# Kernel optimization log

Measured on AMD Instinct MI355X. Metric: run time of the kernel, lower is better.

Reference implementation:

```python
import jax, jax.numpy as jnp
import numpy as np

LN_EPS = 1e-5

def _layernorm(x, gamma, beta):
    mu = jnp.mean(x, axis=-1, keepdims=True)
    var = jnp.mean((x - mu) ** 2, axis=-1, keepdims=True)
    return (x - mu) / jnp.sqrt(var + LN_EPS) * gamma + beta

def setup_inputs() -> dict:
    key = jax.random.key(0)
    ks = jax.random.split(key, 12)
    B, S, D, V, H = 2, 2048, 1024, 32000, 16
    d_ff = 4 * D
    inp = {}
    inp["V"] = jax.random.randint(ks[0], (B, S), 0, V, dtype=jnp.int64)
    inp["num_heads"] = H
    sc = 0.02
    inp["emb"] = jax.random.normal(ks[1], (V, D), dtype=jnp.float32) * sc
    inp["w_o"] = jax.random.normal(ks[2], (D, D), dtype=jnp.float32) * sc
    inp["w1"] = jax.random.normal(ks[3], (D, d_ff), dtype=jnp.float32) * sc
    inp["b1"] = jnp.zeros((d_ff,), dtype=jnp.float32)
    inp["w2"] = jax.random.normal(ks[4], (d_ff, D), dtype=jnp.float32) * sc
    inp["b2"] = jnp.zeros((D,), dtype=jnp.float32)
    inp["gamma1"] = jnp.ones((D,), dtype=jnp.float32)
    inp["beta1"] = jnp.zeros((D,), dtype=jnp.float32)
    inp["gamma2"] = jnp.ones((D,), dtype=jnp.float32)
    inp["beta2"] = jnp.zeros((D,), dtype=jnp.float32)
    return inp

def reference(V, num_heads, emb, w_o, w1, b1, w2, b2, gamma1, beta1, gamma2, beta2):
    # Embedding lookup: [B, S, D]
    x = emb[V]
    B, S, D = x.shape
    hd = D // num_heads
    # NOTE: the original forward never applies w_q/w_k/w_v -- q=k=v=embedding,
    # split per head along the feature dim.
    qh = x.reshape(B, S, num_heads, hd)
    scores = jnp.einsum("bqhd,bkhd->bhqk", qh, qh) / jnp.sqrt(jnp.float32(hd))
    attn = jax.nn.softmax(scores, axis=-1)
    ctx = jnp.einsum("bhqk,bkhd->bqhd", attn, qh).reshape(B, S, D)
    attn_out = ctx @ w_o
    x1 = _layernorm(x + attn_out, gamma1, beta1)
    ff = jax.nn.relu(x1 @ w1 + b1) @ w2 + b2
    return _layernorm(x1 + ff, gamma2, beta2)
```

## Files before the change

kernel.cpp:

```cpp
#include <hip/hip_runtime.h>
#include <hip/hip_bf16.h>

#define B_  2
#define S_  2048
#define D_  1024
#define H_  16
#define HD_ 64
#define DFF 4096
#define NT  (B_ * S_)

typedef __bf16 bf16;
typedef __bf16 bf16x8 __attribute__((ext_vector_type(8)));
typedef __bf16 bf16x4 __attribute__((ext_vector_type(4)));
typedef __bf16 bf16x2 __attribute__((ext_vector_type(2)));
typedef float  f32x4  __attribute__((ext_vector_type(4)));
typedef float  f32x16 __attribute__((ext_vector_type(16)));
typedef int    i32x2  __attribute__((ext_vector_type(2)));

typedef const __attribute__((address_space(1))) unsigned int GLB_U32;
typedef __attribute__((address_space(3))) unsigned int AS3_U32;

__device__ __forceinline__ void gload16(const void* g, void* l) {
    __builtin_amdgcn_global_load_lds((GLB_U32*)g, (AS3_U32*)l, 16, 0, 0);
}

#define MFMA32(A, B, C) __builtin_amdgcn_mfma_f32_32x32x16_bf16(A, B, C, 0, 0, 0)
#define MFMA16(A, B, C) __builtin_amdgcn_mfma_f32_16x16x32_bf16(A, B, C, 0, 0, 0)

__device__ __forceinline__ unsigned pk2(float a, float b) {
    union { bf16x2 v; unsigned u; } t;
    t.v[0] = (bf16)a; t.v[1] = (bf16)b;
    return t.u;
}

#define ATT_SCL 0.18033688011112042f

#define PREP_EMB  (B_ * (S_ / 32) * (D_ / 32))
#define PREP_WO   ((D_ / 32) * (D_ / 32))
#define PREP_W1   ((D_ / 32) * (DFF / 32))
#define PREP_W2   ((DFF / 32) * (D_ / 32))
#define PREP_TOT  (PREP_EMB + PREP_WO + PREP_W1 + PREP_W2)

__device__ __forceinline__ void transcvt_tile(const float* src, bf16* dst,
                                              int R, int C, int tile,
                                              float* tf, int tx, int ty) {
    int tiles_c = C >> 5;
    int r0 = (tile / tiles_c) << 5;
    int c0 = (tile % tiles_c) << 5;
#pragma unroll
    for (int i = 0; i < 4; i++)
        tf[(ty + i * 8) * 33 + tx] = src[(size_t)(r0 + ty + i * 8) * C + c0 + tx];
    __syncthreads();
#pragma unroll
    for (int i = 0; i < 4; i++)
        dst[(size_t)(c0 + ty + i * 8) * R + r0 + tx] = (bf16)tf[tx * 33 + ty + i * 8];
}

__global__ __launch_bounds__(256)
void k_prep(const int* __restrict__ V, const float* __restrict__ emb,
            bf16* __restrict__ xb, bf16* __restrict__ xT,
            const float* __restrict__ w_o, bf16* __restrict__ wobT,
            const float* __restrict__ w1, bf16* __restrict__ w1T,
            const float* __restrict__ w2, bf16* __restrict__ w2T) {
    __shared__ float tf[32 * 33];
    int bidx = blockIdx.x;
    int tx = threadIdx.x & 31, ty = threadIdx.x >> 5;

    if (bidx < PREP_EMB) {
        bf16* tb = (bf16*)tf;
        const int tiles_d = D_ / 32;
        int b   = bidx / ((S_ / 32) * tiles_d);
        int rem = bidx % ((S_ / 32) * tiles_d);
        int ts = rem / tiles_d, td = rem % tiles_d;
        int s0 = ts * 32, d0 = td * 32;
        bf16* xbb = xb + (size_t)b * S_ * D_;
        bf16* dst = xT + (size_t)b * D_ * S_;
#pragma unroll
        for (int i = 0; i < 4; i++) {
            int srow = s0 + ty + i * 8;
            int vid = V[b * S_ + srow];
            bf16 val = (bf16)emb[(size_t)vid * D_ + d0 + tx];
            xbb[(size_t)srow * D_ + d0 + tx] = val;
            tb[(ty + i * 8) * 34 + tx] = val;
        }
        __syncthreads();
#pragma unroll
        for (int i = 0; i < 4; i++)
            dst[(size_t)(d0 + ty + i * 8) * S_ + s0 + tx] = tb[tx * 34 + ty + i * 8];
    } else if (bidx < PREP_EMB + PREP_WO) {
        transcvt_tile(w_o, wobT, D_, D_, bidx - PREP_EMB, tf, tx, ty);
    } else if (bidx < PREP_EMB + PREP_WO + PREP_W1) {
        transcvt_tile(w1, w1T, D_, DFF, bidx - PREP_EMB - PREP_WO, tf, tx, ty);
    } else {
        transcvt_tile(w2, w2T, DFF, D_, bidx - PREP_EMB - PREP_WO - PREP_W1, tf, tx, ty);
    }
}

__global__ __launch_bounds__(256)
void k_attn(const bf16* __restrict__ xb, const bf16* __restrict__ xT,
            bf16* __restrict__ ctxb) {
    __shared__ alignas(16) bf16 Kt[2][64][64];
    __shared__ alignas(16) bf16 Vt[2][64][64];

    int bh = blockIdx.x >> 4;
    int qt = blockIdx.x & 15;
    int b = bh >> 4, h = bh & 15;
    int tid = threadIdx.x;
    int w = tid >> 6, lane = tid & 63;
    int l31 = lane & 31, hi = lane >> 5;

    const bf16* xq = xb + (size_t)b * S_ * D_ + h * HD_;
    const bf16* vT = xT + ((size_t)b * D_ + h * HD_) * S_;

    int q0 = qt * 128 + w * 32;

    bf16x8 qf[4];
#pragma unroll
    for (int c = 0; c < 4; c++) {
        qf[c] = *(const bf16x8*)(xq + (size_t)(q0 + l31) * D_ + c * 16 + hi * 8);
#pragma unroll
        for (int i = 0; i < 8; i++)
            qf[c][i] = (bf16)((float)qf[c][i] * ATT_SCL);
    }

    bf16x8 onesf;
#pragma unroll
    for (int i = 0; i < 8; i++) onesf[i] = (bf16)1.0f;

    int srow = tid >> 3;
    int sbyx = ((tid & 7) << 4) ^ ((srow & 7) << 4);

    const char* kg = (const char*)(xq + (size_t)srow * D_) + sbyx;
    const char* vg = (const char*)(vT + (size_t)srow * S_) + sbyx;
    char* kd0 = (char*)&Kt[0][0][0] + tid * 16;
    char* vd0 = (char*)&Vt[0][0][0] + tid * 16;
    char* kd1 = (char*)&Kt[1][0][0] + tid * 16;
    char* vd1 = (char*)&Vt[1][0][0] + tid * 16;

    f32x16 o0 = {}, o1 = {}, ol = {};

    const int KSTR = 64 * D_ * 2;
    const int VSTR = 64 * 2;
    const int NTILES = S_ / 64;

    gload16(kg, kd0); gload16(kg + 32 * D_ * 2, kd0 + 4096);
    gload16(vg, vd0); gload16(vg + 32 * S_ * 2, vd0 + 4096);
    kg += KSTR; vg += VSTR;

    int rsw = (l31 & 7) << 4;
    const char* KbA = (const char*)&Kt[0][0][0] + l31 * 128;
    const char* KbB = (const char*)&Kt[1][0][0] + l31 * 128;
    const char* VbA = (const char*)&Vt[0][0][0] + l31 * 128;
    const char* VbB = (const char*)&Vt[1][0][0] + l31 * 128;

    for (int kt = 0; kt < NTILES; kt++) {
        __syncthreads();
        if (kt + 1 < NTILES) {
            char* kd = (kt & 1) ? kd0 : kd1;
            char* vd = (kt & 1) ? vd0 : vd1;
            gload16(kg, kd); gload16(kg + 32 * D_ * 2, kd + 4096);
            gload16(vg, vd); gload16(vg + 32 * S_ * 2, vd + 4096);
            kg += KSTR; vg += VSTR;
        }
        const char* Kb = (kt & 1) ? KbB : KbA;
        const char* Vb = (kt & 1) ? VbB : VbA;

        f32x16 sa0 = {}, sa1 = {};
        {
            bf16x8 kf0[4], kf1[4];
#pragma unroll
            for (int c = 0; c < 4; c++) {
                int by = (c * 32 + hi * 16) ^ rsw;
                kf0[c] = *(const bf16x8*)(Kb + by);
                kf1[c] = *(const bf16x8*)(Kb + 32 * 128 + by);
            }
            __builtin_amdgcn_s_setprio(1);
#pragma unroll
            for (int c = 0; c < 4; c++) sa0 = MFMA32(kf0[c], qf[c], sa0);
#pragma unroll
            for (int c = 0; c < 4; c++) sa1 = MFMA32(kf1[c], qf[c], sa1);
            __builtin_amdgcn_s_setprio(0);
        }

        float p0[16], p1[16];
#pragma unroll
        for (int i = 0; i < 16; i++) p0[i] = exp2f(sa0[i]);
#pragma unroll
        for (int i = 0; i < 16; i++) p1[i] = exp2f(sa1[i]);

        union { unsigned u[4]; bf16x8 v; } pfA0, pfA1, pfB0, pfB1;
        {
            unsigned a0 = pk2(p0[0],  p0[1]),  a1 = pk2(p0[2],  p0[3]);
            unsigned a2 = pk2(p0[4],  p0[5]),  a3 = pk2(p0[6],  p0[7]);
            unsigned a4 = pk2(p0[8],  p0[9]),  a5 = pk2(p0[10], p0[11]);
            unsigned a6 = pk2(p0[12], p0[13]), a7 = pk2(p0[14], p0[15]);
            i32x2 r;
            r = __builtin_amdgcn_permlane32_swap((int)a0, (int)a2, false, false);
            pfA0.u[0] = r[0]; pfA0.u[2] = r[1];
            r = __builtin_amdgcn_permlane32_swap((int)a1, (int)a3, false, false);
            pfA0.u[1] = r[0]; pfA0.u[3] = r[1];
            r = __builtin_amdgcn_permlane32_swap((int)a4, (int)a6, false, false);
            pfA1.u[0] = r[0]; pfA1.u[2] = r[1];
            r = __builtin_amdgcn_permlane32_swap((int)a5, (int)a7, false, false);
            pfA1.u[1] = r[0]; pfA1.u[3] = r[1];
        }
        {
            unsigned a0 = pk2(p1[0],  p1[1]),  a1 = pk2(p1[2],  p1[3]);
            unsigned a2 = pk2(p1[4],  p1[5]),  a3 = pk2(p1[6],  p1[7]);
            unsigned a4 = pk2(p1[8],  p1[9]),  a5 = pk2(p1[10], p1[11]);
            unsigned a6 = pk2(p1[12], p1[13]), a7 = pk2(p1[14], p1[15]);
            i32x2 r;
            r = __builtin_amdgcn_permlane32_swap((int)a0, (int)a2, false, false);
            pfB0.u[0] = r[0]; pfB0.u[2] = r[1];
            r = __builtin_amdgcn_permlane32_swap((int)a1, (int)a3, false, false);
            pfB0.u[1] = r[0]; pfB0.u[3] = r[1];
            r = __builtin_amdgcn_permlane32_swap((int)a4, (int)a6, false, false);
            pfB1.u[0] = r[0]; pfB1.u[2] = r[1];
            r = __builtin_amdgcn_permlane32_swap((int)a5, (int)a7, false, false);
            pfB1.u[1] = r[0]; pfB1.u[3] = r[1];
        }

        {
            bf16x8 v0, v1, v2, v3;
            v0 = *(const bf16x8*)(Vb + ((0  + hi * 16) ^ rsw));
            v1 = *(const bf16x8*)(Vb + ((32 + hi * 16) ^ rsw));
            v2 = *(const bf16x8*)(Vb + ((64 + hi * 16) ^ rsw));
            v3 = *(const bf16x8*)(Vb + ((96 + hi * 16) ^ rsw));
            __builtin_amdgcn_s_setprio(1);
            o0 = MFMA32(v0, pfA0.v, o0);
            o0 = MFMA32(v1, pfA1.v, o0);
            o0 = MFMA32(v2, pfB0.v, o0);
            o0 = MFMA32(v3, pfB1.v, o0);
            ol = MFMA32(onesf, pfA0.v, ol);
            ol = MFMA32(onesf, pfA1.v, ol);
            __builtin_amdgcn_s_setprio(0);
            v0 = *(const bf16x8*)(Vb + 32 * 128 + ((0  + hi * 16) ^ rsw));
            v1 = *(const bf16x8*)(Vb + 32 * 128 + ((32 + hi * 16) ^ rsw));
            v2 = *(const bf16x8*)(Vb + 32 * 128 + ((64 + hi * 16) ^ rsw));
            v3 = *(const bf16x8*)(Vb + 32 * 128 + ((96 + hi * 16) ^ rsw));
            __builtin_amdgcn_s_setprio(1);
            o1 = MFMA32(v0, pfA0.v, o1);
            o1 = MFMA32(v1, pfA1.v, o1);
            o1 = MFMA32(v2, pfB0.v, o1);
            o1 = MFMA32(v3, pfB1.v, o1);
            ol = MFMA32(onesf, pfB0.v, ol);
            ol = MFMA32(onesf, pfB1.v, ol);
            __builtin_amdgcn_s_setprio(0);
        }
    }

    float rinv = 1.0f / ol[0];
    int q = q0 + l31;
    bf16* crow = ctxb + ((size_t)b * S_ + q) * D_ + h * HD_;
#pragma unroll
    for (int g = 0; g < 4; g++) {
        bf16x4 ov;
#pragma unroll
        for (int j = 0; j < 4; j++) ov[j] = (bf16)(o0[4 * g + j] * rinv);
        *(bf16x4*)(crow + 8 * g + 4 * hi) = ov;
    }
#pragma unroll
    for (int g = 0; g < 4; g++) {
        bf16x4 ov;
#pragma unroll
        for (int j = 0; j < 4; j++) ov[j] = (bf16)(o1[4 * g + j] * rinv);
        *(bf16x4*)(crow + 32 + 8 * g + 4 * hi) = ov;
    }
}

template <int BIAS, int RELU, int OUT_MODE>
__global__ __launch_bounds__(512)
void k_gemm256(const bf16* __restrict__ A, const bf16* __restrict__ Bt,
               const float* __restrict__ bias,
               float* __restrict__ outf, bf16* __restrict__ outb,
               int M, int N, int K) {
    __shared__ alignas(16) bf16 As[2][256][64];
    __shared__ alignas(16) bf16 Bs[2][256][64];

    int ntn = N >> 8;
    int m0 = (int)(blockIdx.x / ntn) << 8;
    int n0 = (int)(blockIdx.x % ntn) << 8;
    int tid = threadIdx.x;
    int lane = tid & 63, w = tid >> 6;
    int wm = w >> 2, wn = w & 3;
    int l15 = lane & 15, lhi = lane >> 4;
    int NK = K >> 6;

    int r0 = tid >> 3;
    int sbyx = ((tid & 7) << 4) ^ ((r0 & 7) << 4);
    const char* ag = (const char*)(A  + (size_t)(m0 + r0) * K) + sbyx;
    const char* bg = (const char*)(Bt + (size_t)(n0 + r0) * K) + sbyx;
    const size_t r64 = (size_t)64 * K * 2;

    auto stA = [&](int ob, size_t ko, int half) {
        char* d = (char*)&As[ob][0][0] + half * 16384 + tid * 16;
        gload16(ag + ko + (size_t)(2 * half) * r64, d);
        gload16(ag + ko + (size_t)(2 * half + 1) * r64, d + 8192);
    };
    auto stB = [&](int ob, size_t ko, int half) {
        char* d = (char*)&Bs[ob][0][0] + half * 16384 + tid * 16;
        gload16(bg + ko + (size_t)(2 * half) * r64, d);
        gload16(bg + ko + (size_t)(2 * half + 1) * r64, d + 8192);
    };

    stA(0, 0, 0); stA(0, 0, 1); stB(0, 0, 0); stB(0, 0, 1);

    f32x4 acc[8][4] = {};
    int rsw = (l15 & 7) << 4;
    int aro = (wm * 128 + l15) * 128;
    int bro = (wn * 64 + l15) * 128;

    for (int t = 0; t < NK; t++) {
        int buf = t & 1, ob = buf ^ 1;
        size_t ko = (size_t)(t + 1) * 128;
        const char* aB = (const char*)&As[buf][0][0] + aro;
        const char* bB = (const char*)&Bs[buf][0][0] + bro;
        bf16x8 af[4][2], bfr[4][2];

        if (t + 1 < NK) {
            stA(ob, ko, 0); stA(ob, ko, 1);
            asm volatile("s_waitcnt vmcnt(4)" ::: "memory");
        } else {
            asm volatile("s_waitcnt vmcnt(0)" ::: "memory");
        }
        __builtin_amdgcn_s_barrier();
        __builtin_amdgcn_sched_barrier(0);
#pragma unroll
        for (int mi = 0; mi < 4; mi++) {
            af[mi][0] = *(const bf16x8*)(aB + mi * 2048 + ((lhi * 16) ^ rsw));
            af[mi][1] = *(const bf16x8*)(aB + mi * 2048 + ((64 + lhi * 16) ^ rsw));
        }
#pragma unroll
        for (int ni = 0; ni < 2; ni++) {
            bfr[ni][0] = *(const bf16x8*)(bB + ni * 2048 + ((lhi * 16) ^ rsw));
            bfr[ni][1] = *(const bf16x8*)(bB + ni * 2048 + ((64 + lhi * 16) ^ rsw));
        }
        __builtin_amdgcn_s_setprio(1);
#pragma unroll
        for (int mi = 0; mi < 4; mi++)
#pragma unroll
            for (int ni = 0; ni < 2; ni++) {
                acc[mi][ni] = MFMA16(af[mi][0], bfr[ni][0], acc[mi][ni]);
                acc[mi][ni] = MFMA16(af[mi][1], bfr[ni][1], acc[mi][ni]);
            }
        __builtin_amdgcn_s_setprio(0);
        __builtin_amdgcn_s_barrier();

#pragma unroll
        for (int ni = 2; ni < 4; ni++) {
            bfr[ni][0] = *(const bf16x8*)(bB + ni * 2048 + ((lhi * 16) ^ rsw));
            bfr[ni][1] = *(const bf16x8*)(bB + ni * 2048 + ((64 + lhi * 16) ^ rsw));
        }
        if (t + 1 < NK) { stB(ob, ko, 0); stB(ob, ko, 1); }
        __builtin_amdgcn_s_barrier();
        __builtin_amdgcn_s_setprio(1);
#pragma unroll
        for (int mi = 0; mi < 4; mi++)
#pragma unroll
            for (int ni = 2; ni < 4; ni++) {
                acc[mi][ni] = MFMA16(af[mi][0], bfr[ni][0], acc[mi][ni]);
                acc[mi][ni] = MFMA16(af[mi][1], bfr[ni][1], acc[mi][ni]);
            }
        __builtin_amdgcn_s_setprio(0);
        __builtin_amdgcn_s_barrier();

#pragma unroll
        for (int mi = 0; mi < 4; mi++) {
            af[mi][0] = *(const bf16x8*)(aB + (4 + mi) * 2048 + ((lhi * 16) ^ rsw));
            af[mi][1] = *(const bf16x8*)(aB + (4 + mi) * 2048 + ((64 + lhi * 16) ^ rsw));
        }
        __builtin_amdgcn_s_barrier();
        __builtin_amdgcn_s_setprio(1);
#pragma unroll
        for (int mi = 0; mi < 4; mi++)
#pragma unroll
            for (int ni = 0; ni < 2; ni++) {
                acc[4 + mi][ni] = MFMA16(af[mi][0], bfr[ni][0], acc[4 + mi][ni]);
                acc[4 + mi][ni] = MFMA16(af[mi][1], bfr[ni][1], acc[4 + mi][ni]);
            }
        __builtin_amdgcn_s_setprio(0);
        __builtin_amdgcn_s_barrier();

        __builtin_amdgcn_s_barrier();
        __builtin_amdgcn_s_setprio(1);
#pragma unroll
        for (int mi = 0; mi < 4; mi++)
#pragma unroll
            for (int ni = 2; ni < 4; ni++) {
                acc[4 + mi][ni] = MFMA16(af[mi][0], bfr[ni][0], acc[4 + mi][ni]);
                acc[4 + mi][ni] = MFMA16(af[mi][1], bfr[ni][1], acc[4 + mi][ni]);
            }
        __builtin_amdgcn_s_setprio(0);
        __builtin_amdgcn_s_barrier();
    }

#pragma unroll
    for (int mi = 0; mi < 8; mi++) {
        int grow = m0 + wm * 128 + mi * 16 + lhi * 4;
#pragma unroll
        for (int ni = 0; ni < 4; ni++) {
            int gcol = n0 + wn * 64 + ni * 16 + l15;
            float bv = BIAS ? bias[gcol] : 0.f;
#pragma unroll
            for (int r = 0; r < 4; r++) {
                float v = acc[mi][ni][r] + bv;
                if (RELU) v = fmaxf(v, 0.f);
                size_t idx = (size_t)(grow + r) * N + gcol;
                if (OUT_MODE & 1) outf[idx] = v;
                if (OUT_MODE & 2) outb[idx] = (bf16)v;
            }
        }
    }
}

template <int BIAS, int RELU, int OUT_MODE, int SPLITK>
__global__ __launch_bounds__(512)
void k_gemm8(const bf16* __restrict__ A, const bf16* __restrict__ Bt,
             const float* __restrict__ bias,
             float* __restrict__ outf, bf16* __restrict__ outb,
             int M, int N, int K) {
    __shared__ alignas(16) bf16 As[2][256][64];
    __shared__ alignas(16) bf16 Bs[2][128][64];

    int ntn = N >> 7;
    int m0 = (int)(blockIdx.x / ntn) << 8;
    int n0 = (int)(blockIdx.x % ntn) << 7;
    int tid = threadIdx.x;
    int lane = tid & 63;
    int w = tid >> 6;
    int wm = w >> 1, wn = w & 1;
    int l15 = lane & 15, lhi = lane >> 4;

    int Ks = K / SPLITK;
    int NK = Ks >> 6;
    size_t kbase = (size_t)blockIdx.y * Ks;
    float* outp = outf + (size_t)blockIdx.y * M * N;

    int srow = tid >> 3;
    int sbyx = ((tid & 7) << 4) ^ ((srow & 7) << 4);
    const char* ag = (const char*)(A  + (size_t)(m0 + srow) * K + kbase) + sbyx;
    const char* bg = (const char*)(Bt + (size_t)(n0 + srow) * K + kbase) + sbyx;
    const size_t r64 = (size_t)64 * K * 2;

    auto stageA0 = [&](int ob, size_t ko) {
        char* d = (char*)&As[ob][0][0] + tid * 16;
        gload16(ag + ko, d);
        gload16(ag + ko + r64, d + 8192);
    };
    auto stageA1 = [&](int ob, size_t ko) {
        char* d = (char*)&As[ob][0][0] + tid * 16 + 16384;
        gload16(ag + ko + 2 * r64, d);
        gload16(ag + ko + 3 * r64, d + 8192);
    };
    auto stageB = [&](int ob, size_t ko) {
        char* d = (char*)&Bs[ob][0][0] + tid * 16;
        gload16(bg + ko, d);
        gload16(bg + ko + r64, d + 8192);
    };

    stageA0(0, 0); stageA1(0, 0); stageB(0, 0);

    f32x4 acc[4][4] = {};
    int rsw = (l15 & 7) << 4;
    int aro = (wm * 64 + l15) * 128;
    int bro = (wn * 64 + l15) * 128;

    for (int t = 0; t < NK; t++) {
        int buf = t & 1, ob = buf ^ 1;
        size_t ko = (size_t)(t + 1) * 128;
        const char* aB = (const char*)&As[buf][0][0] + aro;
        const char* bB = (const char*)&Bs[buf][0][0] + bro;
        bf16x8 af[4][2], bn[2];

        if (t + 1 < NK) {
            stageA0(ob, ko);
            asm volatile("s_waitcnt vmcnt(2)" ::: "memory");
        } else {
            asm volatile("s_waitcnt vmcnt(0)" ::: "memory");
        }
        __builtin_amdgcn_s_barrier();
#pragma unroll
        for (int m = 0; m < 4; m++) {
            af[m][0] = *(const bf16x8*)(aB + m * 2048 + ((lhi * 16) ^ rsw));
            af[m][1] = *(const bf16x8*)(aB + m * 2048 + ((64 + lhi * 16) ^ rsw));
        }
        bn[0] = *(const bf16x8*)(bB + ((lhi * 16) ^ rsw));
        bn[1] = *(const bf16x8*)(bB + ((64 + lhi * 16) ^ rsw));
        __builtin_amdgcn_s_setprio(1);
#pragma unroll
        for (int m = 0; m < 4; m++) {
            acc[m][0] = MFMA16(af[m][0], bn[0], acc[m][0]);
            acc[m][0] = MFMA16(af[m][1], bn[1], acc[m][0]);
        }
        __builtin_amdgcn_s_setprio(0);
        __builtin_amdgcn_s_barrier();

        bn[0] = *(const bf16x8*)(bB + 2048 + ((lhi * 16) ^ rsw));
        bn[1] = *(const bf16x8*)(bB + 2048 + ((64 + lhi * 16) ^ rsw));
        if (t + 1 < NK) stageA1(ob, ko);
        __builtin_amdgcn_s_barrier();
        __builtin_amdgcn_s_setprio(1);
#pragma unroll
        for (int m = 0; m < 4; m++) {
            acc[m][1] = MFMA16(af[m][0], bn[0], acc[m][1]);
            acc[m][1] = MFMA16(af[m][1], bn[1], acc[m][1]);
        }
        __builtin_amdgcn_s_setprio(0);
        __builtin_amdgcn_s_barrier();

        bn[0] = *(const bf16x8*)(bB + 2 * 2048 + ((lhi * 16) ^ rsw));
        bn[1] = *(const bf16x8*)(bB + 2 * 2048 + ((64 + lhi * 16) ^ rsw));
        if (t + 1 < NK) stageB(ob, ko);
        __builtin_amdgcn_s_barrier();
        __builtin_amdgcn_s_setprio(1);
#pragma unroll
        for (int m = 0; m < 4; m++) {
            acc[m][2] = MFMA16(af[m][0], bn[0], acc[m][2]);
            acc[m][2] = MFMA16(af[m][1], bn[1], acc[m][2]);
        }
        __builtin_amdgcn_s_setprio(0);
        __builtin_amdgcn_s_barrier();

        bn[0] = *(const bf16x8*)(bB + 3 * 2048 + ((lhi * 16) ^ rsw));
        bn[1] = *(const bf16x8*)(bB + 3 * 2048 + ((64 + lhi * 16) ^ rsw));
        __builtin_amdgcn_s_barrier();
        __builtin_amdgcn_s_setprio(1);
#pragma unroll
        for (int m = 0; m < 4; m++) {
            acc[m][3] = MFMA16(af[m][0], bn[0], acc[m][3]);
            acc[m][3] = MFMA16(af[m][1], bn[1], acc[m][3]);
        }
        __builtin_amdgcn_s_setprio(0);
        __builtin_amdgcn_s_barrier();
    }

#pragma unroll
    for (int m = 0; m < 4; m++) {
        int grow = m0 + wm * 64 + m * 16 + lhi * 4;
#pragma unroll
        for (int n = 0; n < 4; n++) {
            int gcol = n0 + wn * 64 + n * 16 + l15;
            float bv = BIAS ? bias[gcol] : 0.f;
#pragma unroll
            for (int r = 0; r < 4; r++) {
                float v = acc[m][n][r] + bv;
                if (RELU) v = fmaxf(v, 0.f);
                size_t idx = (size_t)(grow + r) * N + gcol;
                if (OUT_MODE & 1) outp[idx] = v;
                if (OUT_MODE & 2) outb[idx] = (bf16)v;
            }
        }
    }
}

template <int BIAS, int RELU, int OUT_MODE, int SPLITK>
__global__ __launch_bounds__(256)
void k_gemm(const bf16* __restrict__ A, const bf16* __restrict__ Bt,
            const float* __restrict__ bias,
            float* __restrict__ outf, bf16* __restrict__ outb,
            int M, int N, int K) {
    __shared__ alignas(16) bf16 As[128][32];
    __shared__ alignas(16) bf16 Bs[128][32];

    int nb_n = N >> 7;
    int m0 = (blockIdx.x / nb_n) << 7;
    int n0 = (blockIdx.x % nb_n) << 7;
    int tid = threadIdx.x;
    int w = tid >> 6, lane = tid & 63;
    int wr = (w >> 1) << 6, wc = (w & 1) << 6;
    int l15 = lane & 15, lhi = lane >> 4;

    int srow = w * 16 + (lane >> 2);
    int scol = (lane & 3) << 3;

    int Ks = K / SPLITK;
    int kbase = blockIdx.y * Ks;
    float* outp = outf + (size_t)blockIdx.y * M * N;

    f32x4 acc[4][4] = {};

    for (int k0 = kbase; k0 < kbase + Ks; k0 += 32) {
        gload16(A  + (size_t)(m0 + srow) * K + k0 + scol,      &As[srow][scol]);
        gload16(A  + (size_t)(m0 + 64 + srow) * K + k0 + scol, &As[64 + srow][scol]);
        gload16(Bt + (size_t)(n0 + srow) * K + k0 + scol,      &Bs[srow][scol]);
        gload16(Bt + (size_t)(n0 + 64 + srow) * K + k0 + scol, &Bs[64 + srow][scol]);
        __syncthreads();
        bf16x8 af[4], bfr[4];
#pragma unroll
        for (int mi = 0; mi < 4; mi++)
            af[mi] = *(const bf16x8*)&As[wr + mi * 16 + l15][lhi * 8];
#pragma unroll
        for (int ni = 0; ni < 4; ni++)
            bfr[ni] = *(const bf16x8*)&Bs[wc + ni * 16 + l15][lhi * 8];
#pragma unroll
        for (int mi = 0; mi < 4; mi++)
#pragma unroll
            for (int ni = 0; ni < 4; ni++)
                acc[mi][ni] = MFMA16(af[mi], bfr[ni], acc[mi][ni]);
        __syncthreads();
    }

#pragma unroll
    for (int mi = 0; mi < 4; mi++) {
        int grow = m0 + wr + mi * 16 + lhi * 4;
#pragma unroll
        for (int ni = 0; ni < 4; ni++) {
            int gcol = n0 + wc + ni * 16 + l15;
            float bv = BIAS ? bias[gcol] : 0.f;
#pragma unroll
            for (int r = 0; r < 4; r++) {
                float v = acc[mi][ni][r] + bv;
                if (RELU) v = fmaxf(v, 0.f);
                size_t idx = (size_t)(grow + r) * N + gcol;
                if (OUT_MODE & 1) outp[idx] = v;
                if (OUT_MODE & 2) outb[idx] = (bf16)v;
            }
        }
    }
}

__global__ __launch_bounds__(256)
void k_ln1(const float* __restrict__ pA, const bf16* __restrict__ resb,
           const float* __restrict__ gamma, const float* __restrict__ beta,
           bf16* __restrict__ x1b) {
    const float* pB = pA + (size_t)NT * D_;
    int row = blockIdx.x, tid = threadIdx.x;
    size_t base = (size_t)row * D_ + tid * 4;
    float4 a = *(const float4*)(pA + base);
    float4 c = *(const float4*)(pB + base);
    bf16x4 rb = *(const bf16x4*)(resb + base);
    float4 v;
    v.x = a.x + c.x + (float)rb[0];
    v.y = a.y + c.y + (float)rb[1];
    v.z = a.z + c.z + (float)rb[2];
    v.w = a.w + c.w + (float)rb[3];
    float s  = v.x + v.y + v.z + v.w;
    float sq = v.x * v.x + v.y * v.y + v.z * v.z + v.w * v.w;
#pragma unroll
    for (int m = 1; m < 64; m <<= 1) {
        s  += __shfl_xor(s, m, 64);
        sq += __shfl_xor(sq, m, 64);
    }
    __shared__ float ss[4], ssq[4];
    int w = tid >> 6;
    if ((tid & 63) == 0) { ss[w] = s; ssq[w] = sq; }
    __syncthreads();
    s  = ss[0] + ss[1] + ss[2] + ss[3];
    sq = ssq[0] + ssq[1] + ssq[2] + ssq[3];
    float mu  = s * (1.f / D_);
    float var = sq * (1.f / D_) - mu * mu;
    float rstd = rsqrtf(var + 1e-5f);
    float4 g  = *(const float4*)(gamma + tid * 4);
    float4 bt = *(const float4*)(beta + tid * 4);
    bf16x4 ob;
    ob[0] = (bf16)((v.x - mu) * rstd * g.x + bt.x);
    ob[1] = (bf16)((v.y - mu) * rstd * g.y + bt.y);
    ob[2] = (bf16)((v.z - mu) * rstd * g.z + bt.z);
    ob[3] = (bf16)((v.w - mu) * rstd * g.w + bt.w);
    *(bf16x4*)(x1b + base) = ob;
}

__global__ __launch_bounds__(256)
void k_ln2(const float* __restrict__ pA, const float* __restrict__ bias,
           const bf16* __restrict__ resb,
           const float* __restrict__ gamma, const float* __restrict__ beta,
           float* __restrict__ out) {
    const float* pB = pA + (size_t)NT * D_;
    int row = blockIdx.x, tid = threadIdx.x;
    size_t base = (size_t)row * D_ + tid * 4;
    float4 a = *(const float4*)(pA + base);
    float4 c = *(const float4*)(pB + base);
    bf16x4 rb = *(const bf16x4*)(resb + base);
    float4 bb = *(const float4*)(bias + tid * 4);
    float4 v;
    v.x = a.x + c.x + (float)rb[0] + bb.x;
    v.y = a.y + c.y + (float)rb[1] + bb.y;
    v.z = a.z + c.z + (float)rb[2] + bb.z;
    v.w = a.w + c.w + (float)rb[3] + bb.w;
    float s  = v.x + v.y + v.z + v.w;
    float sq = v.x * v.x + v.y * v.y + v.z * v.z + v.w * v.w;
#pragma unroll
    for (int m = 1; m < 64; m <<= 1) {
        s  += __shfl_xor(s, m, 64);
        sq += __shfl_xor(sq, m, 64);
    }
    __shared__ float ss[4], ssq[4];
    int w = tid >> 6;
    if ((tid & 63) == 0) { ss[w] = s; ssq[w] = sq; }
    __syncthreads();
    s  = ss[0] + ss[1] + ss[2] + ss[3];
    sq = ssq[0] + ssq[1] + ssq[2] + ssq[3];
    float mu  = s * (1.f / D_);
    float var = sq * (1.f / D_) - mu * mu;
    float rstd = rsqrtf(var + 1e-5f);
    float4 g  = *(const float4*)(gamma + tid * 4);
    float4 bt = *(const float4*)(beta + tid * 4);
    float4 o;
    o.x = (v.x - mu) * rstd * g.x + bt.x;
    o.y = (v.y - mu) * rstd * g.y + bt.y;
    o.z = (v.z - mu) * rstd * g.z + bt.z;
    o.w = (v.w - mu) * rstd * g.w + bt.w;
    *(float4*)(out + base) = o;
}

extern "C" void kernel_launch(void* const* d_in, const int* in_sizes, int n_in,
                              void* d_out, int out_size, void* d_ws, size_t ws_size,
                              hipStream_t stream) {
    const int*   Vi  = (const int*)d_in[0];
    const float* emb = (const float*)d_in[2];
    const float* w_o = (const float*)d_in[3];
    const float* w1  = (const float*)d_in[4];
    const float* b1  = (const float*)d_in[5];
    const float* w2  = (const float*)d_in[6];
    const float* b2  = (const float*)d_in[7];
    const float* g1  = (const float*)d_in[8];
    const float* be1 = (const float*)d_in[9];
    const float* g2  = (const float*)d_in[10];
    const float* be2 = (const float*)d_in[11];
    float* out = (float*)d_out;

    char* ws = (char*)d_ws;
    size_t off = 0;
    auto alloc = [&](size_t bytes) -> void* {
        void* p = ws + off;
        off += (bytes + 255) & ~(size_t)255;
        return p;
    };
    bf16*  xb   = (bf16*)alloc((size_t)NT * D_ * 2);
    bf16*  xT   = (bf16*)alloc((size_t)NT * D_ * 2);
    bf16*  wobT = (bf16*)alloc((size_t)D_ * D_ * 2);
    bf16*  w1T  = (bf16*)alloc((size_t)DFF * D_ * 2);
    bf16*  w2T  = (bf16*)alloc((size_t)D_ * DFF * 2);
    bf16*  ctxb = (bf16*)alloc((size_t)NT * D_ * 2);
    bf16*  x1b  = (bf16*)alloc((size_t)NT * D_ * 2);
    bf16*  h1   = (bf16*)alloc((size_t)NT * DFF * 2);
    float* RB   = (float*)alloc((size_t)2 * NT * D_ * 4);
    float* g1p  = RB;
    float* g3p  = RB;

    k_prep<<<PREP_TOT, 256, 0, stream>>>(Vi, emb, xb, xT, w_o, wobT, w1, w1T, w2, w2T);

    k_attn<<<32 * (S_ / 128), 256, 0, stream>>>(xb, xT, ctxb);

    k_gemm<0, 0, 1, 2><<<dim3((NT / 128) * (D_ / 128), 2), 256, 0, stream>>>(
        ctxb, wobT, nullptr, g1p, nullptr, NT, D_, D_);
    k_ln1<<<NT, 256, 0, stream>>>(g1p, xb, g1, be1, x1b);

    k_gemm256<1, 1, 2><<<(NT / 256) * (DFF / 256), 512, 0, stream>>>(
        x1b, w1T, b1, nullptr, h1, NT, DFF, D_);

    k_gemm8<0, 0, 1, 2><<<dim3((NT / 256) * (D_ / 128), 2), 512, 0, stream>>>(
        h1, w2T, nullptr, g3p, nullptr, NT, D_, DFF);
    k_ln2<<<NT, 256, 0, stream>>>(g3p, b2, x1b, g2, be2, out);
}
```

Before: 215.5 us.

## Triple-buffer attention K/V tiles and unify GEMM kernels into two-phase pipeline

The attention kernel moves from double to triple buffering of K/V tiles. It prefetches two tiles ahead and waits with explicit vmcnt instead of a full __syncthreads, to hide more global-load latency. The 512-thread GEMM is restructured from four barrier phases per k-step into two: A loads in one phase and B in the other, with all 16 MFMAs per half-k. The old 128x128 GEMM for the w_o projection is removed, so that projection now uses the same 256x128 kernel. The extra LDS for attention and the larger tile for the w_o GEMM may lower occupancy or leave CUs idle, since that GEMM now has fewer blocks.

```diff
diff --git a/kernel.cpp b/kernel.cpp
--- a/kernel.cpp
+++ b/kernel.cpp
@@ -99,8 +99,8 @@
 __global__ __launch_bounds__(256)
 void k_attn(const bf16* __restrict__ xb, const bf16* __restrict__ xT,
             bf16* __restrict__ ctxb) {
-    __shared__ alignas(16) bf16 Kt[2][64][64];
-    __shared__ alignas(16) bf16 Vt[2][64][64];
+    __shared__ alignas(16) bf16 Kt[3][64][64];
+    __shared__ alignas(16) bf16 Vt[3][64][64];
 
     int bh = blockIdx.x >> 4;
     int qt = blockIdx.x & 15;
@@ -132,38 +132,46 @@
 
     const char* kg = (const char*)(xq + (size_t)srow * D_) + sbyx;
     const char* vg = (const char*)(vT + (size_t)srow * S_) + sbyx;
-    char* kd0 = (char*)&Kt[0][0][0] + tid * 16;
-    char* vd0 = (char*)&Vt[0][0][0] + tid * 16;
-    char* kd1 = (char*)&Kt[1][0][0] + tid * 16;
-    char* vd1 = (char*)&Vt[1][0][0] + tid * 16;
-
-    f32x16 o0 = {}, o1 = {}, ol = {};
+
+    char* kdA = (char*)&Kt[0][0][0] + tid * 16;
+    char* kdB = (char*)&Kt[1][0][0] + tid * 16;
+    char* kdC = (char*)&Kt[2][0][0] + tid * 16;
+    char* vdA = (char*)&Vt[0][0][0] + tid * 16;
+    char* vdB = (char*)&Vt[1][0][0] + tid * 16;
+    char* vdC = (char*)&Vt[2][0][0] + tid * 16;
 
     const int KSTR = 64 * D_ * 2;
     const int VSTR = 64 * 2;
     const int NTILES = S_ / 64;
 
-    gload16(kg, kd0); gload16(kg + 32 * D_ * 2, kd0 + 4096);
-    gload16(vg, vd0); gload16(vg + 32 * S_ * 2, vd0 + 4096);
-    kg += KSTR; vg += VSTR;
+    auto stage = [&](char* kd, char* vd) {
+        gload16(kg, kd); gload16(kg + 32 * D_ * 2, kd + 4096);
+        gload16(vg, vd); gload16(vg + 32 * S_ * 2, vd + 4096);
+        kg += KSTR; vg += VSTR;
+    };
+
+    stage(kdA, vdA);
+    stage(kdB, vdB);
 
     int rsw = (l31 & 7) << 4;
-    const char* KbA = (const char*)&Kt[0][0][0] + l31 * 128;
-    const char* KbB = (const char*)&Kt[1][0][0] + l31 * 128;
-    const char* VbA = (const char*)&Vt[0][0][0] + l31 * 128;
-    const char* VbB = (const char*)&Vt[1][0][0] + l31 * 128;
+    const char* KrA = (const char*)&Kt[0][0][0] + l31 * 128;
+    const char* KrB = (const char*)&Kt[1][0][0] + l31 * 128;
+    const char* KrC = (const char*)&Kt[2][0][0] + l31 * 128;
+    const char* VrA = (const char*)&Vt[0][0][0] + l31 * 128;
+    const char* VrB = (const char*)&Vt[1][0][0] + l31 * 128;
+    const char* VrC = (const char*)&Vt[2][0][0] + l31 * 128;
+
+    f32x16 o0 = {}, o1 = {}, ol = {};
 
     for (int kt = 0; kt < NTILES; kt++) {
-        __syncthreads();
-        if (kt + 1 < NTILES) {
-            char* kd = (kt & 1) ? kd0 : kd1;
-            char* vd = (kt & 1) ? vd0 : vd1;
-            gload16(kg, kd); gload16(kg + 32 * D_ * 2, kd + 4096);
-            gload16(vg, vd); gload16(vg + 32 * S_ * 2, vd + 4096);
-            kg += KSTR; vg += VSTR;
-        }
-        const char* Kb = (kt & 1) ? KbB : KbA;
-        const char* Vb = (kt & 1) ? VbB : VbA;
+        if (kt == NTILES - 1) asm volatile("s_waitcnt vmcnt(0)" ::: "memory");
+        else                  asm volatile("s_waitcnt vmcnt(4)" ::: "memory");
+        __builtin_amdgcn_s_barrier();
+        __builtin_amdgcn_sched_barrier(0);
+        if (kt + 2 < NTILES) stage(kdC, vdC);
+
+        const char* Kb = KrA;
+        const char* Vb = VrA;
 
         f32x16 sa0 = {}, sa1 = {};
         {
@@ -247,6 +255,11 @@
             ol = MFMA32(onesf, pfB1.v, ol);
             __builtin_amdgcn_s_setprio(0);
         }
+
+        const char* tk = KrA; KrA = KrB; KrB = KrC; KrC = tk;
+        const char* tv = VrA; VrA = VrB; VrB = VrC; VrC = tv;
+        char* tk2 = kdA; kdA = kdB; kdB = kdC; kdC = tk2;
+        char* tv2 = vdA; vdA = vdB; vdB = vdC; vdC = tv2;
     }
 
     float rinv = 1.0f / ol[0];
@@ -415,10 +428,10 @@
 
 template <int BIAS, int RELU, int OUT_MODE, int SPLITK>
 __global__ __launch_bounds__(512)
-void k_gemm8(const bf16* __restrict__ A, const bf16* __restrict__ Bt,
-             const float* __restrict__ bias,
-             float* __restrict__ outf, bf16* __restrict__ outb,
-             int M, int N, int K) {
+void k_g2(const bf16* __restrict__ A, const bf16* __restrict__ Bt,
+          const float* __restrict__ bias,
+          float* __restrict__ outf, bf16* __restrict__ outb,
+          int M, int N, int K) {
     __shared__ alignas(16) bf16 As[2][256][64];
     __shared__ alignas(16) bf16 Bs[2][128][64];
 
@@ -426,8 +439,7 @@
     int m0 = (int)(blockIdx.x / ntn) << 8;
     int n0 = (int)(blockIdx.x % ntn) << 7;
     int tid = threadIdx.x;
-    int lane = tid & 63;
-    int w = tid >> 6;
+    int lane = tid & 63, w = tid >> 6;
     int wm = w >> 1, wn = w & 1;
     int l15 = lane & 15, lhi = lane >> 4;
 
@@ -442,23 +454,20 @@
     const char* bg = (const char*)(Bt + (size_t)(n0 + srow) * K + kbase) + sbyx;
     const size_t r64 = (size_t)64 * K * 2;
 
-    auto stageA0 = [&](int ob, size_t ko) {
+    auto stA = [&](int ob, size_t ko) {
         char* d = (char*)&As[ob][0][0] + tid * 16;
         gload16(ag + ko, d);
         gload16(ag + ko + r64, d + 8192);
+        gload16(ag + ko + 2 * r64, d + 16384);
+        gload16(ag + ko + 3 * r64, d + 24576);
     };
-    auto stageA1 = [&](int ob, size_t ko) {
-        char* d = (char*)&As[ob][0][0] + tid * 16 + 16384;
-        gload16(ag + ko + 2 * r64, d);
-        gload16(ag + ko + 3 * r64, d + 8192);
-    };
-    auto stageB = [&](int ob, size_t ko) {
+    auto stB = [&](int ob, size_t ko) {
         char* d = (char*)&Bs[ob][0][0] + tid * 16;
         gload16(bg + ko, d);
         gload16(bg + ko + r64, d + 8192);
     };
 
-    stageA0(0, 0); stageA1(0, 0); stageB(0, 0);
+    stA(0, 0); stB(0, 0);
 
     f32x4 acc[4][4] = {};
     int rsw = (l15 & 7) << 4;
@@ -470,142 +479,55 @@
         size_t ko = (size_t)(t + 1) * 128;
         const char* aB = (const char*)&As[buf][0][0] + aro;
         const char* bB = (const char*)&Bs[buf][0][0] + bro;
-        bf16x8 af[4][2], bn[2];
+        bf16x8 af[4][2], bn[4][2];
 
         if (t + 1 < NK) {
-            stageA0(ob, ko);
-            asm volatile("s_waitcnt vmcnt(2)" ::: "memory");
+            stA(ob, ko);
+            asm volatile("s_waitcnt vmcnt(4)" ::: "memory");
         } else {
             asm volatile("s_waitcnt vmcnt(0)" ::: "memory");
         }
         __builtin_amdgcn_s_barrier();
-#pragma unroll
-        for (int m = 0; m < 4; m++) {
-            af[m][0] = *(const bf16x8*)(aB + m * 2048 + ((lhi * 16) ^ rsw));
-            af[m][1] = *(const bf16x8*)(aB + m * 2048 + ((64 + lhi * 16) ^ rsw));
-        }
-        bn[0] = *(const bf16x8*)(bB + ((lhi * 16) ^ rsw));
-        bn[1] = *(const bf16x8*)(bB + ((64 + lhi * 16) ^ rsw));
+        __builtin_amdgcn_sched_barrier(0);
+#pragma unroll
+        for (int mi = 0; mi < 4; mi++)
+            af[mi][0] = *(const bf16x8*)(aB + mi * 2048 + ((lhi * 16) ^ rsw));
+#pragma unroll
+        for (int ni = 0; ni < 4; ni++)
+            bn[ni][0] = *(const bf16x8*)(bB + ni * 2048 + ((lhi * 16) ^ rsw));
         __builtin_amdgcn_s_setprio(1);
 #pragma unroll
-        for (int m = 0; m < 4; m++) {
-            acc[m][0] = MFMA16(af[m][0], bn[0], acc[m][0]);
-            acc[m][0] = MFMA16(af[m][1], bn[1], acc[m][0]);
-        }
+        for (int mi = 0; mi < 4; mi++)
+#pragma unroll
+            for (int ni = 0; ni < 4; ni++)
+                acc[mi][ni] = MFMA16(af[mi][0], bn[ni][0], acc[mi][ni]);
         __builtin_amdgcn_s_setprio(0);
         __builtin_amdgcn_s_barrier();
 
-        bn[0] = *(const bf16x8*)(bB + 2048 + ((lhi * 16) ^ rsw));
-        bn[1] = *(const bf16x8*)(bB + 2048 + ((64 + lhi * 16) ^ rsw));
-        if (t + 1 < NK) stageA1(ob, ko);
+#pragma unroll
+        for (int mi = 0; mi < 4; mi++)
+            af[mi][1] = *(const bf16x8*)(aB + mi * 2048 + ((64 + lhi * 16) ^ rsw));
+#pragma unroll
+        for (int ni = 0; ni < 4; ni++)
+            bn[ni][1] = *(const bf16x8*)(bB + ni * 2048 + ((64 + lhi * 16) ^ rsw));
+        if (t + 1 < NK) stB(ob, ko);
         __builtin_amdgcn_s_barrier();
         __builtin_amdgcn_s_setprio(1);
 #pragma unroll
-        for (int m = 0; m < 4; m++) {
-            acc[m][1] = MFMA16(af[m][0], bn[0], acc[m][1]);
-            acc[m][1] = MFMA16(af[m][1], bn[1], acc[m][1]);
-        }
+        for (int mi = 0; mi < 4; mi++)
+#pragma unroll
+            for (int ni = 0; ni < 4; ni++)
+                acc[mi][ni] = MFMA16(af[mi][1], bn[ni][1], acc[mi][ni]);
         __builtin_amdgcn_s_setprio(0);
         __builtin_amdgcn_s_barrier();
-
-        bn[0] = *(const bf16x8*)(bB + 2 * 2048 + ((lhi * 16) ^ rsw));
-        bn[1] = *(const bf16x8*)(bB + 2 * 2048 + ((64 + lhi * 16) ^ rsw));
-        if (t + 1 < NK) stageB(ob, ko);
-        __builtin_amdgcn_s_barrier();
-        __builtin_amdgcn_s_setprio(1);
-#pragma unroll
-        for (int m = 0; m < 4; m++) {
-            acc[m][2] = MFMA16(af[m][0], bn[0], acc[m][2]);
-            acc[m][2] = MFMA16(af[m][1], bn[1], acc[m][2]);
-        }
-        __builtin_amdgcn_s_setprio(0);
-        __builtin_amdgcn_s_barrier();
-
-        bn[0] = *(const bf16x8*)(bB + 3 * 2048 + ((lhi * 16) ^ rsw));
-        bn[1] = *(const bf16x8*)(bB + 3 * 2048 + ((64 + lhi * 16) ^ rsw));
-        __builtin_amdgcn_s_barrier();
-        __builtin_amdgcn_s_setprio(1);
-#pragma unroll
-        for (int m = 0; m < 4; m++) {
-            acc[m][3] = MFMA16(af[m][0], bn[0], acc[m][3]);
-            acc[m][3] = MFMA16(af[m][1], bn[1], acc[m][3]);
-        }
-        __builtin_amdgcn_s_setprio(0);
-        __builtin_amdgcn_s_barrier();
-    }
-
-#pragma unroll
-    for (int m = 0; m < 4; m++) {
-        int grow = m0 + wm * 64 + m * 16 + lhi * 4;
-#pragma unroll
-        for (int n = 0; n < 4; n++) {
-            int gcol = n0 + wn * 64 + n * 16 + l15;
-            float bv = BIAS ? bias[gcol] : 0.f;
-#pragma unroll
-            for (int r = 0; r < 4; r++) {
-                float v = acc[m][n][r] + bv;
-                if (RELU) v = fmaxf(v, 0.f);
-                size_t idx = (size_t)(grow + r) * N + gcol;
-                if (OUT_MODE & 1) outp[idx] = v;
-                if (OUT_MODE & 2) outb[idx] = (bf16)v;
-            }
-        }
-    }
-}
-
-template <int BIAS, int RELU, int OUT_MODE, int SPLITK>
-__global__ __launch_bounds__(256)
-void k_gemm(const bf16* __restrict__ A, const bf16* __restrict__ Bt,
-            const float* __restrict__ bias,
-            float* __restrict__ outf, bf16* __restrict__ outb,
-            int M, int N, int K) {
-    __shared__ alignas(16) bf16 As[128][32];
-    __shared__ alignas(16) bf16 Bs[128][32];
-
-    int nb_n = N >> 7;
-    int m0 = (blockIdx.x / nb_n) << 7;
-    int n0 = (blockIdx.x % nb_n) << 7;
-    int tid = threadIdx.x;
-    int w = tid >> 6, lane = tid & 63;
-    int wr = (w >> 1) << 6, wc = (w & 1) << 6;
-    int l15 = lane & 15, lhi = lane >> 4;
-
-    int srow = w * 16 + (lane >> 2);
-    int scol = (lane & 3) << 3;
-
-    int Ks = K / SPLITK;
-    int kbase = blockIdx.y * Ks;
-    float* outp = outf + (size_t)blockIdx.y * M * N;
-
-    f32x4 acc[4][4] = {};
-
-    for (int k0 = kbase; k0 < kbase + Ks; k0 += 32) {
-        gload16(A  + (size_t)(m0 + srow) * K + k0 + scol,      &As[srow][scol]);
-        gload16(A  + (size_t)(m0 + 64 + srow) * K + k0 + scol, &As[64 + srow][scol]);
-        gload16(Bt + (size_t)(n0 + srow) * K + k0 + scol,      &Bs[srow][scol]);
-        gload16(Bt + (size_t)(n0 + 64 + srow) * K + k0 + scol, &Bs[64 + srow][scol]);
-        __syncthreads();
-        bf16x8 af[4], bfr[4];
-#pragma unroll
-        for (int mi = 0; mi < 4; mi++)
-            af[mi] = *(const bf16x8*)&As[wr + mi * 16 + l15][lhi * 8];
-#pragma unroll
-        for (int ni = 0; ni < 4; ni++)
-            bfr[ni] = *(const bf16x8*)&Bs[wc + ni * 16 + l15][lhi * 8];
-#pragma unroll
-        for (int mi = 0; mi < 4; mi++)
-#pragma unroll
-            for (int ni = 0; ni < 4; ni++)
-                acc[mi][ni] = MFMA16(af[mi], bfr[ni], acc[mi][ni]);
-        __syncthreads();
     }
 
 #pragma unroll
     for (int mi = 0; mi < 4; mi++) {
-        int grow = m0 + wr + mi * 16 + lhi * 4;
+        int grow = m0 + wm * 64 + mi * 16 + lhi * 4;
 #pragma unroll
         for (int ni = 0; ni < 4; ni++) {
-            int gcol = n0 + wc + ni * 16 + l15;
+            int gcol = n0 + wn * 64 + ni * 16 + l15;
             float bv = BIAS ? bias[gcol] : 0.f;
 #pragma unroll
             for (int r = 0; r < 4; r++) {
@@ -742,14 +664,14 @@
 
     k_attn<<<32 * (S_ / 128), 256, 0, stream>>>(xb, xT, ctxb);
 
-    k_gemm<0, 0, 1, 2><<<dim3((NT / 128) * (D_ / 128), 2), 256, 0, stream>>>(
+    k_g2<0, 0, 1, 2><<<dim3((NT / 256) * (D_ / 128), 2), 512, 0, stream>>>(
         ctxb, wobT, nullptr, g1p, nullptr, NT, D_, D_);
     k_ln1<<<NT, 256, 0, stream>>>(g1p, xb, g1, be1, x1b);
 
     k_gemm256<1, 1, 2><<<(NT / 256) * (DFF / 256), 512, 0, stream>>>(
         x1b, w1T, b1, nullptr, h1, NT, DFF, D_);
 
-    k_gemm8<0, 0, 1, 2><<<dim3((NT / 256) * (D_ / 128), 2), 512, 0, stream>>>(
+    k_g2<0, 0, 1, 2><<<dim3((NT / 256) * (D_ / 128), 2), 512, 0, stream>>>(
         h1, w2T, nullptr, g3p, nullptr, NT, D_, DFF);
     k_ln2<<<NT, 256, 0, stream>>>(g3p, b2, x1b, g2, be2, out);
 }
```

New measurement: 208.4 us. 1.03x faster.
